# Optimization experiments

Measured on AMD Instinct MI355X. Metric: run time of the kernel, lower is better.

Reference implementation:

```python
import jax, jax.numpy as jnp
from jax import lax
import numpy as np

# ---- static config (matches init_kwargs) ----
B, H, W = 8, 32, 32
L = H * W                      # 1024 tokens
D_MODEL = 384
MAMBA_DIM = 192                # d_model * d_mamba_ratio
LOCAL_DIM = 192
D_INNER = 384                  # expand_m * MAMBA_DIM
D_STATE = 16
D_CONV = 4
DT_RANK = 12                   # ceil(MAMBA_DIM / 16)
NDIR = 4                       # h, h_flip, v, v_flip
RED = 48                       # int(D_INNER * 0.125), BiAttn reduce dim
INNER_C = 192                  # LOCAL_DIM * expand_c
K_C = 8                        # local block depthwise kernel size


def setup_inputs() -> dict:
    key = jax.random.key(0)
    ks = jax.random.split(key, 16)
    s = 0.02
    return {
        "x": jax.random.normal(ks[0], (B, L, D_MODEL), jnp.float32),
        "in_proj_w": jax.random.normal(ks[1], (2 * D_INNER, MAMBA_DIM)) * s,
        "A_log": jnp.broadcast_to(jnp.log(jnp.arange(1, D_STATE + 1, dtype=jnp.float32)), (NDIR, D_INNER, D_STATE)) + 0.0,
        "conv_w": jax.random.normal(ks[2], (NDIR, D_INNER, D_CONV)) * 0.2,
        "conv_b": jax.random.normal(ks[3], (NDIR, D_INNER)) * 0.02,
        "xproj_w": jax.random.normal(ks[4], (NDIR, DT_RANK + 2 * D_STATE, D_INNER)) * s,
        "dtproj_w": jax.random.normal(ks[5], (NDIR, D_INNER, DT_RANK)) * (DT_RANK ** -0.5),
        "dtproj_b": jax.random.normal(ks[6], (NDIR, D_INNER)) * 0.5 - 4.0,
        "Dp": jnp.ones((NDIR, D_INNER)),
        "out_proj_w": jax.random.normal(ks[7], (MAMBA_DIM, D_INNER)) * s,
        "attn_ln_g": jnp.ones((D_INNER,)),
        "attn_ln_b": jnp.zeros((D_INNER,)),
        "attn_gr_w": jax.random.normal(ks[8], (RED, D_INNER)) * s,
        "attn_gr_b": jnp.zeros((RED,)),
        "attn_cs_w": jax.random.normal(ks[9], (D_INNER, RED)) * s,
        "attn_cs_b": jnp.zeros((D_INNER,)),
        "pw1_w": jax.random.normal(ks[10], (2 * INNER_C, LOCAL_DIM)) * s,
        "pw1_b": jnp.zeros((2 * INNER_C,)),
        "dw_w": jax.random.normal(ks[11], (INNER_C, K_C)) * 0.2,
        "dw_b": jnp.zeros((INNER_C,)),
        "bn_g": jnp.ones((INNER_C,)),
        "bn_b": jnp.zeros((INNER_C,)),
        "pw2_w": jax.random.normal(ks[12], (LOCAL_DIM, INNER_C)) * s,
        "pw2_b": jnp.zeros((LOCAL_DIM,)),
    }


def _forward(x, in_proj_w, A_log, conv_w, conv_b, xproj_w, dtproj_w, dtproj_b, Dp,
             out_proj_w, attn_ln_g, attn_ln_b, attn_gr_w, attn_gr_b, attn_cs_w, attn_cs_b,
             pw1_w, pw1_b, dw_w, dw_b, bn_g, bn_b, pw2_w, pw2_b):
    mamba_in = x[:, :, :MAMBA_DIM]
    local_in = x[:, :, MAMBA_DIM:]

    # ---------- MultiMamba branch ----------
    xz = jnp.swapaxes(mamba_in @ in_proj_w.T, 1, 2)   # (B, 2*D_INNER, L)

    def to_dir(t, i):
        # reorder channel-last-token axis per scan direction
        if i == 0:
            return t
        if i == 1:
            return jnp.flip(t, -1)
        tv = t.reshape(B, -1, H, W).swapaxes(-1, -2).reshape(B, -1, L)  # column-major scan
        return tv if i == 2 else jnp.flip(tv, -1)

    def from_dir(t, i):
        if i == 0:
            return t
        if i == 1:
            return jnp.flip(t, -1)
        if i == 3:
            t = jnp.flip(t, -1)
        return t.reshape(B, -1, W, H).swapaxes(-1, -2).reshape(B, -1, L)

    def ssm_dir(xzd, i):
        # mamba_inner_fn_no_out_proj: causal dwconv -> silu -> x_proj -> selective scan -> gate
        xp, z = jnp.split(xzd, 2, axis=1)            # (B, D_INNER, L) each
        xpad = jnp.pad(xp, ((0, 0), (0, 0), (D_CONV - 1, 0)))
        u = lax.conv_general_dilated(xpad, conv_w[i][:, None, :], (1,), 'VALID',
                                     dimension_numbers=('NCH', 'OIH', 'NCH'),
                                     feature_group_count=D_INNER)
        u = jax.nn.silu(u + conv_b[i][None, :, None])
        dbl = jnp.einsum('bdl,rd->brl', u, xproj_w[i])
        dt = dbl[:, :DT_RANK]
        Bm = dbl[:, DT_RANK:DT_RANK + D_STATE]
        Cm = dbl[:, DT_RANK + D_STATE:]
        delta = jax.nn.softplus(jnp.einsum('brl,dr->bdl', dt, dtproj_w[i]) + dtproj_b[i][None, :, None])
        A = -jnp.exp(A_log[i])                        # (D_INNER, D_STATE)

        def step(h, inps):
            d_t, B_t, C_t, u_t = inps                 # (B,d),(B,n),(B,n),(B,d)
            h = jnp.exp(d_t[:, :, None] * A) * h + (d_t * u_t)[:, :, None] * B_t[:, None, :]
            return h, jnp.einsum('bdn,bn->bd', h, C_t)

        h0 = jnp.zeros((B, D_INNER, D_STATE), x.dtype)
        _, ys = lax.scan(step, h0, (delta.transpose(2, 0, 1), Bm.transpose(2, 0, 1),
                                    Cm.transpose(2, 0, 1), u.transpose(2, 0, 1)))
        y = ys.transpose(1, 2, 0) + u * Dp[i][:, None]  # (B, D_INNER, L)
        return y * jax.nn.silu(z)

    def biattn(t):                                     # (B, L, D_INNER)
        mu = t.mean(-1, keepdims=True)
        var = ((t - mu) ** 2).mean(-1, keepdims=True)
        tn = (t - mu) / jnp.sqrt(var + 1e-5) * attn_ln_g + attn_ln_b
        g = tn.mean(1, keepdims=True)                  # global pool (B,1,D_INNER)
        g = jax.nn.gelu(g @ attn_gr_w.T + attn_gr_b, approximate=False)
        c = jax.nn.sigmoid(g @ attn_cs_w.T + attn_cs_b)
        return t * c

    acc = jnp.zeros((B, L, D_INNER), x.dtype)
    for i in range(NDIR):                              # fixed small set of directions
        out_i = from_dir(ssm_dir(to_dir(xz, i), i), i)
        acc = acc + biattn(jnp.swapaxes(out_i, 1, 2))
    mamba_out = acc @ out_proj_w.T                     # (B, L, MAMBA_DIM)

    # ---------- Local conv branch ----------
    hch = jnp.einsum('blc,oc->bol', local_in, pw1_w) + pw1_b[None, :, None]
    a, gte = jnp.split(hch, 2, axis=1)
    hch = a * jax.nn.sigmoid(gte)                      # GLU, (B, INNER_C, L)
    pad_l = K_C // 2
    pad_r = K_C // 2 - (K_C + 1) % 2                   # calc_same_padding(8) -> (4, 3)
    hpad = jnp.pad(hch, ((0, 0), (0, 0), (pad_l, pad_r)))
    hch = lax.conv_general_dilated(hpad, dw_w[:, None, :], (1,), 'VALID',
                                   dimension_numbers=('NCH', 'OIH', 'NCH'),
                                   feature_group_count=INNER_C) + dw_b[None, :, None]
    mu = hch.mean((0, 2))                              # BatchNorm1d (training-mode batch stats)
    var = hch.var((0, 2))
    hch = (hch - mu[None, :, None]) / jnp.sqrt(var + 1e-5)[None, :, None] * bn_g[None, :, None] + bn_b[None, :, None]
    hch = hch * jax.nn.sigmoid(hch)                    # Swish
    local_out = jnp.einsum('bcl,oc->blo', hch, pw2_w) + pw2_b

    return jnp.concatenate([mamba_out, local_out], axis=-1)


def reference(x, in_proj_w, A_log, conv_w, conv_b, xproj_w, dtproj_w, dtproj_b, Dp,
              out_proj_w, attn_ln_g, attn_ln_b, attn_gr_w, attn_gr_b, attn_cs_w, attn_cs_b,
              pw1_w, pw1_b, dw_w, dw_b, bn_g, bn_b, pw2_w, pw2_b):
    return _forward(x, in_proj_w, A_log, conv_w, conv_b, xproj_w, dtproj_w, dtproj_b, Dp,
                    out_proj_w, attn_ln_g, attn_ln_b, attn_gr_w, attn_gr_b, attn_cs_w, attn_cs_b,
                    pw1_w, pw1_b, dw_w, dw_b, bn_g, bn_b, pw2_w, pw2_b)
```

## Files before the change

kernel.cpp:

```cpp
#include <hip/hip_runtime.h>
#include <stdint.h>


#define DEV __device__ __forceinline__

typedef __attribute__((ext_vector_type(8))) short short8;
typedef __attribute__((ext_vector_type(4))) short short4v;
typedef __attribute__((ext_vector_type(4))) float f32x4;

DEV float bf(ushort v) { union { uint32_t u; float f; } c; c.u = ((uint32_t)v) << 16; return c.f; }
DEV ushort fbf(float f) {
  union { float f; uint32_t u; } c; c.f = f;
  uint32_t u = c.u;
  return (ushort)((u + 0x7FFFu + ((u >> 16) & 1u)) >> 16);
}

#if __has_builtin(__builtin_amdgcn_exp2f)
DEV float fexp2(float x) { return __builtin_amdgcn_exp2f(x); }
#else
DEV float fexp2(float x) { return __expf(x * 0.6931471805599453f); }
#endif

template<int CTRL>
DEV float rradd(float x) {
  return x + __int_as_float(__builtin_amdgcn_update_dpp(
      0, __float_as_int(x), CTRL, 0xF, 0xF, true));
}

DEV int pmap(int i, int j) {
  if (i == 0) return j;
  if (i == 1) return 1023 - j;
  if (i == 2) return ((j & 31) << 5) | (j >> 5);
  int k = 1023 - j; return ((k & 31) << 5) | (k >> 5);
}

DEV void cvt4(const float* __restrict__ s, ushort* __restrict__ d, int blk, int tid) {
  const int idx = (blk * 256 + tid) * 4;
  float4 v = *(const float4*)(s + idx);
  d[idx] = fbf(v.x); d[idx + 1] = fbf(v.y); d[idx + 2] = fbf(v.z); d[idx + 3] = fbf(v.w);
}

__global__ __launch_bounds__(256) void prep_all(
    const float* __restrict__ x, ushort* __restrict__ xb,
    const float* __restrict__ ipw, ushort* __restrict__ ipwb,
    const float* __restrict__ opw, ushort* __restrict__ opwb,
    const float* __restrict__ pw1w, ushort* __restrict__ pw1wb,
    const float* __restrict__ pw2w, ushort* __restrict__ pw2wb,
    const float* __restrict__ xw, ushort* __restrict__ xwp)
{
  const int bx = blockIdx.x, tid = threadIdx.x;
  if (bx < 3072)      cvt4(x, xb, bx, tid);
  else if (bx < 3216) cvt4(ipw, ipwb, bx - 3072, tid);
  else if (bx < 3288) cvt4(opw, opwb, bx - 3216, tid);
  else if (bx < 3360) cvt4(pw1w, pw1wb, bx - 3288, tid);
  else if (bx < 3396) cvt4(pw2w, pw2wb, bx - 3360, tid);
  else {
    const int row = bx - 3396;
    const int i = row >> 6, nn = row & 63;
    for (int c = tid; c < 384; c += 256)
      xwp[(size_t)row * 384 + c] = (nn < 44) ? fbf(xw[((size_t)i * 44 + nn) * 384 + c]) : (ushort)0;
  }
}

template<bool BF16OUT, bool BIAS>
__global__ __launch_bounds__(256) void gemm_bt(
    const ushort* __restrict__ A, long long sAz, int lda,
    const ushort* __restrict__ Bw, long long sBz,
    const float* __restrict__ bias,
    void* __restrict__ C, long long sCz, int ldc, int coff, int K)
{
  __shared__ ushort As[64][40];
  __shared__ ushort Bs[64][40];
  A += (size_t)blockIdx.z * sAz;
  Bw += (size_t)blockIdx.z * sBz;
  const int tid = threadIdx.x;
  const int m0 = blockIdx.x * 64, n0 = blockIdx.y * 64;
  const int w = tid >> 6, lane = tid & 63, l15 = lane & 15, quad = lane >> 4;
  const int sr = tid >> 2, sc = (tid & 3) * 8;
  f32x4 acc[4] = {};
  for (int k0 = 0; k0 < K; k0 += 32) {
    __syncthreads();
    *(short8*)&As[sr][sc] = *(const short8*)(A + (size_t)(m0 + sr) * lda + k0 + sc);
    *(short8*)&Bs[sr][sc] = *(const short8*)(Bw + (size_t)(n0 + sr) * K + k0 + sc);
    __syncthreads();
    short8 av = *(short8*)&As[w * 16 + l15][quad * 8];
#pragma unroll
    for (int nt = 0; nt < 4; nt++) {
      short8 bv = *(short8*)&Bs[nt * 16 + l15][quad * 8];
      acc[nt] = __builtin_amdgcn_mfma_f32_16x16x32_bf16(av, bv, acc[nt], 0, 0, 0);
    }
  }
  float* cf = (float*)C + (size_t)blockIdx.z * sCz;
  ushort* cb = (ushort*)C + (size_t)blockIdx.z * sCz;
#pragma unroll
  for (int nt = 0; nt < 4; nt++) {
    const int col = n0 + nt * 16 + l15;
    const float bv = BIAS ? bias[col] : 0.f;
#pragma unroll
    for (int r = 0; r < 4; r++) {
      const int row = m0 + w * 16 + quad * 4 + r;
      float v = acc[nt][r] + bv;
      if (BF16OUT) cb[(size_t)row * ldc + coff + col] = fbf(v);
      else         cf[(size_t)row * ldc + coff + col] = v;
    }
  }
}

__global__ __launch_bounds__(256) void gemm_dual(
    const ushort* __restrict__ A0, int lda0, const ushort* __restrict__ B0,
    const float* __restrict__ bias0, void* __restrict__ C0, int ldc0, int coff0, int K0,
    int nt0, int bf0,
    const ushort* __restrict__ A1, int lda1, const ushort* __restrict__ B1,
    const float* __restrict__ bias1, void* __restrict__ C1, int ldc1, int coff1, int K1,
    int bf1)
{
  __shared__ ushort As[64][40];
  __shared__ ushort Bs[64][40];
  const ushort* A; const ushort* Bw; const float* bias; void* C;
  int lda, ldc, coff, K, bf16o, n0;
  if ((int)blockIdx.y < nt0) {
    A = A0; lda = lda0; Bw = B0; bias = bias0; C = C0; ldc = ldc0; coff = coff0; K = K0;
    bf16o = bf0; n0 = blockIdx.y * 64;
  } else {
    A = A1; lda = lda1; Bw = B1; bias = bias1; C = C1; ldc = ldc1; coff = coff1; K = K1;
    bf16o = bf1; n0 = (blockIdx.y - nt0) * 64;
  }
  const int tid = threadIdx.x;
  const int m0 = blockIdx.x * 64;
  const int w = tid >> 6, lane = tid & 63, l15 = lane & 15, quad = lane >> 4;
  const int sr = tid >> 2, sc = (tid & 3) * 8;
  f32x4 acc[4] = {};
  for (int k0 = 0; k0 < K; k0 += 32) {
    __syncthreads();
    *(short8*)&As[sr][sc] = *(const short8*)(A + (size_t)(m0 + sr) * lda + k0 + sc);
    *(short8*)&Bs[sr][sc] = *(const short8*)(Bw + (size_t)(n0 + sr) * K + k0 + sc);
    __syncthreads();
    short8 av = *(short8*)&As[w * 16 + l15][quad * 8];
#pragma unroll
    for (int nt = 0; nt < 4; nt++) {
      short8 bv = *(short8*)&Bs[nt * 16 + l15][quad * 8];
      acc[nt] = __builtin_amdgcn_mfma_f32_16x16x32_bf16(av, bv, acc[nt], 0, 0, 0);
    }
  }
#pragma unroll
  for (int nt = 0; nt < 4; nt++) {
    const int col = n0 + nt * 16 + l15;
    const float bv = bias ? bias[col] : 0.f;
#pragma unroll
    for (int r = 0; r < 4; r++) {
      const int row = m0 + w * 16 + quad * 4 + r;
      float v = acc[nt][r] + bv;
      if (bf16o) ((ushort*)C)[(size_t)row * ldc + coff + col] = fbf(v);
      else       ((float*)C)[(size_t)row * ldc + coff + col] = v;
    }
  }
}

__global__ __launch_bounds__(384) void conv2_kernel(const ushort* __restrict__ xzb,
    const float* __restrict__ cw, const float* __restrict__ cb, ushort* __restrict__ u)
{
  const int d = threadIdx.x;
  const int jt = blockIdx.x;
  const int b = blockIdx.y, i = blockIdx.z;
  __shared__ ushort sx[35][384];
  const int j0 = jt * 32;
#pragma unroll 5
  for (int r = 0; r < 35; r++) {
    const int jj = j0 - 3 + r;
    sx[r][d] = (jj >= 0) ? xzb[(size_t)((b << 10) + pmap(i, jj)) * 768 + d] : (ushort)0;
  }
  __syncthreads();
  const float w0 = cw[((i * 384 + d) << 2) + 0];
  const float w1 = cw[((i * 384 + d) << 2) + 1];
  const float w2 = cw[((i * 384 + d) << 2) + 2];
  const float w3 = cw[((i * 384 + d) << 2) + 3];
  const float cbv = cb[i * 384 + d];
  ushort* ur = u + ((size_t)((i * 8 + b) << 10) + j0) * 384 + d;
#pragma unroll 4
  for (int q = 0; q < 32; q++) {
    float s = bf(sx[q][d]) * w0 + bf(sx[q + 1][d]) * w1 + bf(sx[q + 2][d]) * w2
            + bf(sx[q + 3][d]) * w3 + cbv;
    ur[(size_t)q * 384] = fbf(s / (1.f + __expf(-s)));
  }
}

#define NCH 16
#define CJ 64
__global__ __launch_bounds__(256, 3) void scan8_kernel(
    const ushort* __restrict__ u,
    const float*  __restrict__ dbl,
    const ushort* __restrict__ xzb,
    const float* __restrict__ alog, const float* __restrict__ dtw,
    const float* __restrict__ dtb, const float* __restrict__ Dpw,
    ushort* __restrict__ y)
{
  const int dt0 = blockIdx.x * NCH;
  const int b = blockIdx.y, i = blockIdx.z;
  const int tid = threadIdx.x;
  const int ch = tid >> 4, n = tid & 15;
  const int d = dt0 + ch;
  const int srow = tid >> 2, role = tid & 3;

  __shared__ float sdt[CJ][13];
  __shared__ float su[CJ][20];
  __shared__ float sz[CJ][20];
  __shared__ float sbc[CJ / 2][68];
  __shared__ float sdu[CJ / 2][68];
  __shared__ float sy[CJ][20];
  __shared__ float sDp[NCH];

  float w48[4][12], dtbv4[4];
#pragma unroll
  for (int cc = 0; cc < 4; cc++) {
    const int chp = 4 * role + cc;
#pragma unroll
    for (int r = 0; r < 12; r++) w48[cc][r] = dtw[((size_t)i * 384 + dt0 + chp) * 12 + r];
    dtbv4[cc] = dtb[i * 384 + dt0 + chp];
  }
  const float L2E = 1.4426950408889634f;
  const float Al = -__expf(alog[((size_t)i * 384 + d) * 16 + n]) * L2E;
  if (tid < NCH) sDp[tid] = Dpw[i * 384 + dt0 + tid];

  const float selm[4] = { (n >> 2) == 0 ? 1.f : 0.f, (n >> 2) == 1 ? 1.f : 0.f,
                          (n >> 2) == 2 ? 1.f : 0.f, (n >> 2) == 3 ? 1.f : 0.f };

  const size_t rb = (size_t)(i * 8 + b) << 10;
  const ushort* ub = u + rb * 384 + dt0;
  const float* dblb = dbl + rb * 64;
  const ushort* zb = xzb + ((size_t)b << 10) * 768 + 384 + dt0;
  ushort* yb = y + rb * 384 + dt0;
  const float* sdup = &sdu[0][4 * ch];
  const float* sbcp = &sbc[0][4 * n];

  float h = 0.f;

  for (int c = 0; c < 16; c++) {
    const int j0 = c * CJ;
    __syncthreads();
    {
      const float* src = dblb + (size_t)(j0 + srow) * 64 + role * 12;
      f32x4 r0 = *(const f32x4*)(src);
      f32x4 r1 = *(const f32x4*)(src + 4);
      f32x4 r2 = *(const f32x4*)(src + 8);
      if (role == 0) {
#pragma unroll
        for (int k = 0; k < 4; k++) {
          sdt[srow][k] = r0[k]; sdt[srow][4 + k] = r1[k]; sdt[srow][8 + k] = r2[k];
        }
      } else {
        float vals[12];
#pragma unroll
        for (int k = 0; k < 4; k++) { vals[k] = r0[k]; vals[4 + k] = r1[k]; vals[8 + k] = r2[k]; }
#pragma unroll
        for (int k = 0; k < 12; k++) {
          const int f = role * 12 + k;
          if (f < 44) {
            const int isC = (f >= 28) ? 1 : 0;
            const int nn = isC ? (f - 28) : (f - 12);
            sbc[srow >> 1][4 * nn + 2 * (srow & 1) + isC] = vals[k];
          }
        }
      }
    }
    {
      const short4v u4 = *(const short4v*)(ub + (size_t)(j0 + srow) * 384 + 4 * role);
      const int lo = pmap(i, j0 + srow);
      const short4v z4 = *(const short4v*)(zb + (size_t)lo * 768 + 4 * role);
      f32x4 uf, zf;
#pragma unroll
      for (int k = 0; k < 4; k++) { uf[k] = bf((ushort)u4[k]); zf[k] = bf((ushort)z4[k]); }
      *(f32x4*)&su[srow][4 * role] = uf;
      *(f32x4*)&sz[srow][4 * role] = zf;
    }
    __syncthreads();
    {
      float dtr[12];
#pragma unroll
      for (int k = 0; k < 12; k++) dtr[k] = sdt[srow][k];
#pragma unroll
      for (int cc = 0; cc < 4; cc++) {
        const int chp = 4 * role + cc;
        float s = dtbv4[cc];
#pragma unroll
        for (int r = 0; r < 12; r++) s += dtr[r] * w48[cc][r];
        const float dl = fmaxf(s, 0.f) + __logf(1.f + __expf(-fabsf(s)));
        float2 pr; pr.x = dl; pr.y = dl * su[srow][chp];
        *(float2*)&sdu[srow >> 1][4 * chp + 2 * (srow & 1)] = pr;
      }
    }
    __syncthreads();
#pragma unroll
    for (int q = 0; q < 4; q++) {
      f32x4 pq = {0.f, 0.f, 0.f, 0.f};
#pragma unroll
      for (int s2 = 0; s2 < 8; s2++) {
        const f32x4 duP = *(const f32x4*)(sdup + (q * 8 + s2) * 68);
        const f32x4 bcP = *(const f32x4*)(sbcp + (q * 8 + s2) * 68);
        {
          const float e = fexp2(duP[0] * Al);
          h = e * h + duP[1] * bcP[0];
          float p = h * bcP[1];
          p = rradd<0x124>(p); p = rradd<0x128>(p);
          pq[s2 >> 1] = fmaf(selm[(2 * s2) & 3], p, pq[s2 >> 1]);
        }
        {
          const float e = fexp2(duP[2] * Al);
          h = e * h + duP[3] * bcP[2];
          float p = h * bcP[3];
          p = rradd<0x124>(p); p = rradd<0x128>(p);
          pq[s2 >> 1] = fmaf(selm[(2 * s2 + 1) & 3], p, pq[s2 >> 1]);
        }
      }
#pragma unroll
      for (int j = 0; j < 4; j++) {
        float t2 = rradd<0xB1>(pq[j]);
        t2 = rradd<0x4E>(t2);
        if ((n & 3) == 0) sy[(q << 4) | (j << 2) | (n >> 2)][ch] = t2;
      }
    }
    __syncthreads();
    {
      const int lo = pmap(i, j0 + srow);
      const f32x4 y4 = *(const f32x4*)&sy[srow][role * 4];
      const f32x4 u4 = *(const f32x4*)&su[srow][role * 4];
      const f32x4 z4 = *(const f32x4*)&sz[srow][role * 4];
      short4v o;
#pragma unroll
      for (int t = 0; t < 4; t++) {
        const float z = z4[t];
        const float val = (y4[t] + u4[t] * sDp[role * 4 + t]) * (z / (1.f + __expf(-z)));
        o[t] = (short)fbf(val);
      }
      *(short4v*)(yb + (size_t)lo * 384 + role * 4) = o;
    }
  }
}

__global__ __launch_bounds__(256) void lngm_kernel(const ushort* __restrict__ y,
                                                   float* __restrict__ G16)
{
  const int slab = blockIdx.x, b = blockIdx.y, i = blockIdx.z;
  const int tid = threadIdx.x;
  const int w = tid >> 6, lane = tid & 63;
  __shared__ float smu[64], srs[64];
  const size_t base = (size_t)i * 8192 + b * 1024 + slab * 64;
  for (int rr = 0; rr < 16; rr++) {
    const int r = w * 16 + rr;
    const ushort* yr = y + (base + r) * 384;
    float s = 0.f, ss = 0.f;
    const short4v v4 = *(const short4v*)(yr + 4 * lane);
    const uint32_t v2 = *(const uint32_t*)(yr + 256 + 2 * lane);
#pragma unroll
    for (int t = 0; t < 4; t++) { float v = bf((ushort)v4[t]); s += v; ss += v * v; }
    { float v = bf((ushort)(v2 & 0xffffu)); s += v; ss += v * v; }
    { float v = bf((ushort)(v2 >> 16));     s += v; ss += v * v; }
#pragma unroll
    for (int off = 1; off < 64; off <<= 1) { s += __shfl_xor(s, off, 64); ss += __shfl_xor(ss, off, 64); }
    if (lane == 0) {
      float m = s * (1.f / 384.f);
      float va = ss * (1.f / 384.f) - m * m;
      smu[r] = m;
      srs[r] = rsqrtf(va + 1e-5f);
    }
  }
  __syncthreads();
  for (int col = tid; col < 384; col += 256) {
    float s = 0.f;
    for (int r = 0; r < 64; r++)
      s += (bf(y[(base + r) * 384 + col]) - smu[r]) * srs[r];
    G16[((size_t)(i * 8 + b) * 16 + slab) * 384 + col] = s;
  }
}

__global__ __launch_bounds__(64) void gate_kernel(const float* __restrict__ G16,
    const float* __restrict__ lng, const float* __restrict__ lnb,
    const float* __restrict__ grw, const float* __restrict__ grb,
    const float* __restrict__ csw, const float* __restrict__ csb, float* __restrict__ cbuf)
{
  const int b = blockIdx.x, i = blockIdx.y;
  const int ib = i * 8 + b;
  const int lane = threadIdx.x;
  __shared__ float sG[384];
  __shared__ float g48[48];
  for (int dd = lane; dd < 384; dd += 64) {
    const float* g = G16 + (size_t)ib * 16 * 384 + dd;
    float s = 0.f;
#pragma unroll
    for (int k = 0; k < 16; k++) s += g[k * 384];
    sG[dd] = s * (1.f / 1024.f) * lng[dd] + lnb[dd];
  }
  __syncthreads();
  if (lane < 48) {
    float s = grb[lane];
    for (int dd = 0; dd < 384; dd++) s += sG[dd] * grw[lane * 384 + dd];
    g48[lane] = 0.5f * s * (1.f + erff(s * 0.70710678118f));
  }
  __syncthreads();
  for (int dd = lane; dd < 384; dd += 64) {
    float s = csb[dd];
#pragma unroll
    for (int r = 0; r < 48; r++) s += g48[r] * csw[dd * 48 + r];
    cbuf[(size_t)ib * 384 + dd] = 1.f / (1.f + __expf(-s));
  }
}

__global__ __launch_bounds__(384) void accgate_kernel(const ushort* __restrict__ y,
    const float* __restrict__ cbuf, ushort* __restrict__ accb)
{
  const int t = threadIdx.x;
  const int row = blockIdx.x * 4 + (t / 96);
  const int cg = (t % 96) * 4;
  const int b = row >> 10;
  f32x4 s = {};
#pragma unroll
  for (int i = 0; i < 4; i++) {
    const short4v v = *(const short4v*)(y + ((size_t)i * 8192 + row) * 384 + cg);
    const f32x4 cv = *(const f32x4*)(cbuf + (size_t)(i * 8 + b) * 384 + cg);
#pragma unroll
    for (int k = 0; k < 4; k++) s[k] += bf((ushort)v[k]) * cv[k];
  }
  short4v o;
#pragma unroll
  for (int k = 0; k < 4; k++) o[k] = (short)fbf(s[k]);
  *(short4v*)(accb + (size_t)row * 384 + cg) = o;
}

__global__ __launch_bounds__(192) void gludwbn_kernel(const ushort* __restrict__ hchb,
    const float* __restrict__ dww, const float* __restrict__ dwb,
    float* __restrict__ h2, float* __restrict__ bnsum)
{
  const int c = threadIdx.x;
  const int lt = blockIdx.x, b = blockIdx.y;
  __shared__ float sv[39][192];
  const int l0 = lt * 32;
#pragma unroll 4
  for (int r = 0; r < 39; r++) {
    const int ls = l0 + r - 4;
    float v = 0.f;
    if (ls >= 0 && ls < 1024) {
      const size_t rr = (size_t)((b << 10) + ls) * 384;
      const float a = bf(hchb[rr + c]);
      const float g = bf(hchb[rr + 192 + c]);
      v = a / (1.f + __expf(-g));
    }
    sv[r][c] = v;
  }
  __syncthreads();
  float wk[8];
#pragma unroll
  for (int k = 0; k < 8; k++) wk[k] = dww[(c << 3) + k];
  const float bias = dwb[c];
  float sacc = 0.f, ssacc = 0.f;
  for (int q = 0; q < 32; q++) {
    float s = bias;
#pragma unroll
    for (int k = 0; k < 8; k++) s += sv[q + k][c] * wk[k];
    h2[(size_t)((b << 10) + l0 + q) * 192 + c] = s;
    sacc += s; ssacc += s * s;
  }
  atomicAdd(&bnsum[c], sacc);
  atomicAdd(&bnsum[192 + c], ssacc);
}

__global__ void bnact_kernel(const float* __restrict__ h2, const float* __restrict__ bnsum,
                             const float* __restrict__ bng, const float* __restrict__ bnb,
                             ushort* __restrict__ sbuf)
{
  const int c = threadIdx.x;
  const int row = blockIdx.x;
  float m = bnsum[c] * (1.f / 8192.f);
  float va = bnsum[192 + c] * (1.f / 8192.f) - m * m;
  float x = (h2[(size_t)row * 192 + c] - m) * rsqrtf(va + 1e-5f) * bng[c] + bnb[c];
  sbuf[(size_t)row * 192 + c] = fbf(x / (1.f + __expf(-x)));
}

extern "C" void kernel_launch(void* const* d_in, const int* in_sizes, int n_in,
                              void* d_out, int out_size, void* d_ws, size_t ws_size,
                              hipStream_t stream) {
  const float* x    = (const float*)d_in[0];
  const float* ipw  = (const float*)d_in[1];
  const float* alog = (const float*)d_in[2];
  const float* cw   = (const float*)d_in[3];
  const float* cbv  = (const float*)d_in[4];
  const float* xw   = (const float*)d_in[5];
  const float* dtw  = (const float*)d_in[6];
  const float* dtb  = (const float*)d_in[7];
  const float* Dpw  = (const float*)d_in[8];
  const float* opw  = (const float*)d_in[9];
  const float* lng  = (const float*)d_in[10];
  const float* lnb  = (const float*)d_in[11];
  const float* grw  = (const float*)d_in[12];
  const float* grb  = (const float*)d_in[13];
  const float* csw  = (const float*)d_in[14];
  const float* csb  = (const float*)d_in[15];
  const float* pw1w = (const float*)d_in[16];
  const float* pw1b = (const float*)d_in[17];
  const float* dww  = (const float*)d_in[18];
  const float* dwb  = (const float*)d_in[19];
  const float* bng  = (const float*)d_in[20];
  const float* bnb  = (const float*)d_in[21];
  const float* pw2w = (const float*)d_in[22];
  const float* pw2b = (const float*)d_in[23];
  float* out = (float*)d_out;

  char* ws = (char*)d_ws;
  ushort* xb    = (ushort*)(ws + 0);
  ushort* xzb   = (ushort*)(ws + 6291456);
  ushort* u     = (ushort*)(ws + 18874368);
  float*  dbl   = (float*)(ws + 44040192);
  ushort* y     = (ushort*)(ws + 52428800);
  ushort* accb  = (ushort*)(ws + 77594624);
  float*  G16   = (float*)(ws + 83886080);
  float*  cbuf  = (float*)(ws + 84672512);
  ushort* xwp   = (ushort*)(ws + 84721664);
  ushort* ipwb  = (ushort*)(ws + 84918272);
  ushort* opwb  = (ushort*)(ws + 85213184);
  ushort* pw1wb = (ushort*)(ws + 85360640);
  ushort* pw2wb = (ushort*)(ws + 85508096);
  float*  bnsum = (float*)(ws + 85581824);
  ushort* hchb = (ushort*)(ws + 18874368);
  float*  h2   = (float*)(ws + 34603008);
  ushort* sbuf = (ushort*)(ws + 40894464);

  prep_all<<<dim3(3652), 256, 0, stream>>>(x, xb, ipw, ipwb, opw, opwb,
                                           pw1w, pw1wb, pw2w, pw2wb, xw, xwp);
  gemm_bt<true, false><<<dim3(128, 12, 1), 256, 0, stream>>>(
      xb, 0, 384, ipwb, 0, nullptr, xzb, 0, 768, 0, 192);
  conv2_kernel<<<dim3(32, 8, 4), 384, 0, stream>>>(xzb, cw, cbv, u);
  gemm_bt<false, false><<<dim3(128, 1, 4), 256, 0, stream>>>(
      u, 8192LL * 384, 384, xwp, 64LL * 384, nullptr, dbl, 8192LL * 64, 64, 0, 384);
  scan8_kernel<<<dim3(24, 8, 4), 256, 0, stream>>>(u, dbl, xzb, alog, dtw, dtb, Dpw, y);
  lngm_kernel<<<dim3(16, 8, 4), 256, 0, stream>>>(y, G16);
  gate_kernel<<<dim3(8, 4), 64, 0, stream>>>(G16, lng, lnb, grw, grb, csw, csb, cbuf);
  accgate_kernel<<<dim3(2048), 384, 0, stream>>>(y, cbuf, accb);
  gemm_dual<<<dim3(128, 9), 256, 0, stream>>>(
      accb, 384, opwb, nullptr, out, 384, 0, 384, 3, 0,
      xb + 192, 384, pw1wb, pw1b, hchb, 384, 0, 192, 1);
  (void)hipMemsetAsync(bnsum, 0, 384 * sizeof(float), stream);
  gludwbn_kernel<<<dim3(32, 8), 192, 0, stream>>>(hchb, dww, dwb, h2, bnsum);
  bnact_kernel<<<dim3(8192), 192, 0, stream>>>(h2, bnsum, bng, bnb, sbuf);
  gemm_bt<false, true><<<dim3(128, 3, 1), 256, 0, stream>>>(
      sbuf, 0, 192, pw2wb, 0, pw2b, out, 0, 384, 192, 192);
}
```

Baseline: 333.9 us.

## Prefetch scan chunk inputs into registers and fuse BN+Swish into pw2 GEMM

The selective-scan kernel now loads the next chunk's dt/B/C, u and z values into registers during the current chunk's recurrence. It keeps u and z in registers rather than staging them through shared memory, which removes two barriers and three shared arrays per chunk. Separately, the BatchNorm-apply plus Swish kernel is folded into the A-tile load of a new pw2 GEMM, which drops one launch and the bf16 intermediate round trip. In exchange, register pressure in the scan kernel rises, and the BN/Swish work is repeated for each of the three N-column blocks.

```diff
diff --git a/kernel.cpp b/kernel.cpp
--- a/kernel.cpp
+++ b/kernel.cpp
@@ -152,6 +152,62 @@
       float v = acc[nt][r] + bv;
       if (bf16o) ((ushort*)C)[(size_t)row * ldc + coff + col] = fbf(v);
       else       ((float*)C)[(size_t)row * ldc + coff + col] = v;
+    }
+  }
+}
+
+__global__ __launch_bounds__(256) void gemm_pw2(
+    const float* __restrict__ h2, const float* __restrict__ bnsum,
+    const float* __restrict__ bng, const float* __restrict__ bnb,
+    const ushort* __restrict__ Bw, const float* __restrict__ bias,
+    float* __restrict__ C)
+{
+  __shared__ ushort As[64][40];
+  __shared__ ushort Bs[64][40];
+  __shared__ float bsc[192], bsh[192];
+  const int tid = threadIdx.x;
+  const int m0 = blockIdx.x * 64, n0 = blockIdx.y * 64;
+  const int w = tid >> 6, lane = tid & 63, l15 = lane & 15, quad = lane >> 4;
+  const int sr = tid >> 2, sc = (tid & 3) * 8;
+  for (int cth = tid; cth < 192; cth += 256) {
+    float m = bnsum[cth] * (1.f / 8192.f);
+    float va = bnsum[192 + cth] * (1.f / 8192.f) - m * m;
+    float s = bng[cth] * rsqrtf(va + 1e-5f);
+    bsc[cth] = s; bsh[cth] = bnb[cth] - m * s;
+  }
+  f32x4 acc[4] = {};
+  for (int k0 = 0; k0 < 192; k0 += 32) {
+    __syncthreads();
+    {
+      const float* hr = h2 + (size_t)(m0 + sr) * 192 + k0 + sc;
+      f32x4 a0 = *(const f32x4*)(hr);
+      f32x4 a1 = *(const f32x4*)(hr + 4);
+      short8 v;
+#pragma unroll
+      for (int k = 0; k < 8; k++) {
+        const float xx = (k < 4) ? a0[k] : a1[k - 4];
+        const float xn = xx * bsc[k0 + sc + k] + bsh[k0 + sc + k];
+        v[k] = (short)fbf(xn / (1.f + __expf(-xn)));
+      }
+      *(short8*)&As[sr][sc] = v;
+    }
+    *(short8*)&Bs[sr][sc] = *(const short8*)(Bw + (size_t)(n0 + sr) * 192 + k0 + sc);
+    __syncthreads();
+    short8 av = *(short8*)&As[w * 16 + l15][quad * 8];
+#pragma unroll
+    for (int nt = 0; nt < 4; nt++) {
+      short8 bv = *(short8*)&Bs[nt * 16 + l15][quad * 8];
+      acc[nt] = __builtin_amdgcn_mfma_f32_16x16x32_bf16(av, bv, acc[nt], 0, 0, 0);
+    }
+  }
+#pragma unroll
+  for (int nt = 0; nt < 4; nt++) {
+    const int col = n0 + nt * 16 + l15;
+    const float bv = bias[col];
+#pragma unroll
+    for (int r = 0; r < 4; r++) {
+      const int row = m0 + w * 16 + quad * 4 + r;
+      C[(size_t)row * 384 + 192 + col] = acc[nt][r] + bv;
     }
   }
 }
@@ -186,7 +242,7 @@
 
 #define NCH 16
 #define CJ 64
-__global__ __launch_bounds__(256, 3) void scan8_kernel(
+__global__ __launch_bounds__(256, 3) void scan9_kernel(
     const ushort* __restrict__ u,
     const float*  __restrict__ dbl,
     const ushort* __restrict__ xzb,
@@ -198,12 +254,8 @@
   const int b = blockIdx.y, i = blockIdx.z;
   const int tid = threadIdx.x;
   const int ch = tid >> 4, n = tid & 15;
-  const int d = dt0 + ch;
   const int srow = tid >> 2, role = tid & 3;
 
-  __shared__ float sdt[CJ][13];
-  __shared__ float su[CJ][20];
-  __shared__ float sz[CJ][20];
   __shared__ float sbc[CJ / 2][68];
   __shared__ float sdu[CJ / 2][68];
   __shared__ float sy[CJ][20];
@@ -218,7 +270,7 @@
     dtbv4[cc] = dtb[i * 384 + dt0 + chp];
   }
   const float L2E = 1.4426950408889634f;
-  const float Al = -__expf(alog[((size_t)i * 384 + d) * 16 + n]) * L2E;
+  const float Al = -__expf(alog[((size_t)i * 384 + dt0 + ch) * 16 + n]) * L2E;
   if (tid < NCH) sDp[tid] = Dpw[i * 384 + dt0 + tid];
 
   const float selm[4] = { (n >> 2) == 0 ? 1.f : 0.f, (n >> 2) == 1 ? 1.f : 0.f,
@@ -232,63 +284,62 @@
   const float* sdup = &sdu[0][4 * ch];
   const float* sbcp = &sbc[0][4 * n];
 
+  f32x4 nd0, nd1, nd2, ns0, ns1, ns2; short4v nu, nz;
+  {
+    const float* src = dblb + (size_t)srow * 64;
+    nd0 = *(const f32x4*)(src); nd1 = *(const f32x4*)(src + 4); nd2 = *(const f32x4*)(src + 8);
+    const float* seg = src + role * 12;
+    ns0 = *(const f32x4*)(seg); ns1 = *(const f32x4*)(seg + 4); ns2 = *(const f32x4*)(seg + 8);
+    nu = *(const short4v*)(ub + (size_t)srow * 384 + 4 * role);
+    nz = *(const short4v*)(zb + (size_t)pmap(i, srow) * 768 + 4 * role);
+  }
+
   float h = 0.f;
 
   for (int c = 0; c < 16; c++) {
     const int j0 = c * CJ;
-    __syncthreads();
-    {
-      const float* src = dblb + (size_t)(j0 + srow) * 64 + role * 12;
-      f32x4 r0 = *(const f32x4*)(src);
-      f32x4 r1 = *(const f32x4*)(src + 4);
-      f32x4 r2 = *(const f32x4*)(src + 8);
-      if (role == 0) {
-#pragma unroll
-        for (int k = 0; k < 4; k++) {
-          sdt[srow][k] = r0[k]; sdt[srow][4 + k] = r1[k]; sdt[srow][8 + k] = r2[k];
-        }
-      } else {
-        float vals[12];
-#pragma unroll
-        for (int k = 0; k < 4; k++) { vals[k] = r0[k]; vals[4 + k] = r1[k]; vals[8 + k] = r2[k]; }
-#pragma unroll
-        for (int k = 0; k < 12; k++) {
-          const int f = role * 12 + k;
-          if (f < 44) {
-            const int isC = (f >= 28) ? 1 : 0;
-            const int nn = isC ? (f - 28) : (f - 12);
-            sbc[srow >> 1][4 * nn + 2 * (srow & 1) + isC] = vals[k];
-          }
+    f32x4 uf, zf;
+#pragma unroll
+    for (int k = 0; k < 4; k++) { uf[k] = bf((ushort)nu[k]); zf[k] = bf((ushort)nz[k]); }
+    if (role != 0) {
+      float vals[12];
+#pragma unroll
+      for (int k = 0; k < 4; k++) { vals[k] = ns0[k]; vals[4 + k] = ns1[k]; vals[8 + k] = ns2[k]; }
+#pragma unroll
+      for (int k = 0; k < 12; k++) {
+        const int f = role * 12 + k;
+        if (f < 44) {
+          const int isC = (f >= 28) ? 1 : 0;
+          const int nn = isC ? (f - 28) : (f - 12);
+          sbc[srow >> 1][4 * nn + 2 * (srow & 1) + isC] = vals[k];
         }
       }
     }
     {
-      const short4v u4 = *(const short4v*)(ub + (size_t)(j0 + srow) * 384 + 4 * role);
-      const int lo = pmap(i, j0 + srow);
-      const short4v z4 = *(const short4v*)(zb + (size_t)lo * 768 + 4 * role);
-      f32x4 uf, zf;
-#pragma unroll
-      for (int k = 0; k < 4; k++) { uf[k] = bf((ushort)u4[k]); zf[k] = bf((ushort)z4[k]); }
-      *(f32x4*)&su[srow][4 * role] = uf;
-      *(f32x4*)&sz[srow][4 * role] = zf;
-    }
-    __syncthreads();
-    {
       float dtr[12];
 #pragma unroll
-      for (int k = 0; k < 12; k++) dtr[k] = sdt[srow][k];
+      for (int k = 0; k < 4; k++) { dtr[k] = nd0[k]; dtr[4 + k] = nd1[k]; dtr[8 + k] = nd2[k]; }
 #pragma unroll
       for (int cc = 0; cc < 4; cc++) {
-        const int chp = 4 * role + cc;
         float s = dtbv4[cc];
 #pragma unroll
         for (int r = 0; r < 12; r++) s += dtr[r] * w48[cc][r];
         const float dl = fmaxf(s, 0.f) + __logf(1.f + __expf(-fabsf(s)));
-        float2 pr; pr.x = dl; pr.y = dl * su[srow][chp];
-        *(float2*)&sdu[srow >> 1][4 * chp + 2 * (srow & 1)] = pr;
+        float2 pr; pr.x = dl; pr.y = dl * uf[cc];
+        *(float2*)&sdu[srow >> 1][4 * (4 * role + cc) + 2 * (srow & 1)] = pr;
       }
     }
     __syncthreads();
+    {
+      const int cn = (c < 15) ? (c + 1) : 0;
+      const int rown = cn * CJ + srow;
+      const float* src = dblb + (size_t)rown * 64;
+      nd0 = *(const f32x4*)(src); nd1 = *(const f32x4*)(src + 4); nd2 = *(const f32x4*)(src + 8);
+      const float* seg = src + role * 12;
+      ns0 = *(const f32x4*)(seg); ns1 = *(const f32x4*)(seg + 4); ns2 = *(const f32x4*)(seg + 8);
+      nu = *(const short4v*)(ub + (size_t)rown * 384 + 4 * role);
+      nz = *(const short4v*)(zb + (size_t)pmap(i, rown) * 768 + 4 * role);
+    }
 #pragma unroll
     for (int q = 0; q < 4; q++) {
       f32x4 pq = {0.f, 0.f, 0.f, 0.f};
@@ -322,13 +373,11 @@
     {
       const int lo = pmap(i, j0 + srow);
       const f32x4 y4 = *(const f32x4*)&sy[srow][role * 4];
-      const f32x4 u4 = *(const f32x4*)&su[srow][role * 4];
-      const f32x4 z4 = *(const f32x4*)&sz[srow][role * 4];
       short4v o;
 #pragma unroll
       for (int t = 0; t < 4; t++) {
-        const float z = z4[t];
-        const float val = (y4[t] + u4[t] * sDp[role * 4 + t]) * (z / (1.f + __expf(-z)));
+        const float z = zf[t];
+        const float val = (y4[t] + uf[t] * sDp[role * 4 + t]) * (z / (1.f + __expf(-z)));
         o[t] = (short)fbf(val);
       }
       *(short4v*)(yb + (size_t)lo * 384 + role * 4) = o;
@@ -460,18 +509,6 @@
   }
   atomicAdd(&bnsum[c], sacc);
   atomicAdd(&bnsum[192 + c], ssacc);
-}
-
-__global__ void bnact_kernel(const float* __restrict__ h2, const float* __restrict__ bnsum,
-                             const float* __restrict__ bng, const float* __restrict__ bnb,
-                             ushort* __restrict__ sbuf)
-{
-  const int c = threadIdx.x;
-  const int row = blockIdx.x;
-  float m = bnsum[c] * (1.f / 8192.f);
-  float va = bnsum[192 + c] * (1.f / 8192.f) - m * m;
-  float x = (h2[(size_t)row * 192 + c] - m) * rsqrtf(va + 1e-5f) * bng[c] + bnb[c];
-  sbuf[(size_t)row * 192 + c] = fbf(x / (1.f + __expf(-x)));
 }
 
 extern "C" void kernel_launch(void* const* d_in, const int* in_sizes, int n_in,
@@ -520,7 +557,6 @@
   float*  bnsum = (float*)(ws + 85581824);
   ushort* hchb = (ushort*)(ws + 18874368);
   float*  h2   = (float*)(ws + 34603008);
-  ushort* sbuf = (ushort*)(ws + 40894464);
 
   prep_all<<<dim3(3652), 256, 0, stream>>>(x, xb, ipw, ipwb, opw, opwb,
                                            pw1w, pw1wb, pw2w, pw2wb, xw, xwp);
@@ -529,7 +565,7 @@
   conv2_kernel<<<dim3(32, 8, 4), 384, 0, stream>>>(xzb, cw, cbv, u);
   gemm_bt<false, false><<<dim3(128, 1, 4), 256, 0, stream>>>(
       u, 8192LL * 384, 384, xwp, 64LL * 384, nullptr, dbl, 8192LL * 64, 64, 0, 384);
-  scan8_kernel<<<dim3(24, 8, 4), 256, 0, stream>>>(u, dbl, xzb, alog, dtw, dtb, Dpw, y);
+  scan9_kernel<<<dim3(24, 8, 4), 256, 0, stream>>>(u, dbl, xzb, alog, dtw, dtb, Dpw, y);
   lngm_kernel<<<dim3(16, 8, 4), 256, 0, stream>>>(y, G16);
   gate_kernel<<<dim3(8, 4), 64, 0, stream>>>(G16, lng, lnb, grw, grb, csw, csb, cbuf);
   accgate_kernel<<<dim3(2048), 384, 0, stream>>>(y, cbuf, accb);
@@ -538,7 +574,5 @@
       xb + 192, 384, pw1wb, pw1b, hchb, 384, 0, 192, 1);
   (void)hipMemsetAsync(bnsum, 0, 384 * sizeof(float), stream);
   gludwbn_kernel<<<dim3(32, 8), 192, 0, stream>>>(hchb, dww, dwb, h2, bnsum);
-  bnact_kernel<<<dim3(8192), 192, 0, stream>>>(h2, bnsum, bng, bnb, sbuf);
-  gemm_bt<false, true><<<dim3(128, 3, 1), 256, 0, stream>>>(
-      sbuf, 0, 192, pw2wb, 0, pw2b, out, 0, 384, 192, 192);
-}
+  gemm_pw2<<<dim3(128, 3), 256, 0, stream>>>(h2, bnsum, bng, bnb, pw2wb, pw2b, out);
+}
```

Result: faster. 324.3 us (-2.9%).
